# Optimization experiments

Hardware: AMD Instinct MI355X
Metric: run time of the kernel (lower is better)

Reference implementation:

```python
import jax, jax.numpy as jnp
import numpy as np


def setup_inputs() -> dict:
    key = jax.random.key(0)
    ks = jax.random.split(key, 6)
    B, S, D_IN, D_OUT, E, R = 4, 2048, 4096, 4096, 8, 16
    x = jax.random.normal(ks[0], (B, S, D_IN), dtype=jnp.float32)
    probs = jax.random.uniform(ks[1], (B, E), dtype=jnp.float32)
    router_probs = probs / jnp.sum(probs, axis=-1, keepdims=True)
    weight = jax.random.normal(ks[2], (D_OUT, D_IN), dtype=jnp.float32) * 0.02
    bias = jax.random.normal(ks[3], (D_OUT,), dtype=jnp.float32) * 0.02
    lora_A = jax.random.normal(ks[4], (E, R, D_IN), dtype=jnp.float32) * 0.02
    lora_B = jax.random.normal(ks[5], (E, D_OUT, R), dtype=jnp.float32) * 0.02
    return {"x": x, "router_probs": router_probs, "weight": weight,
            "bias": bias, "lora_A": lora_A, "lora_B": lora_B}


def reference(x, router_probs, weight, bias, lora_A, lora_B):
    scaling = 2.0
    # base linear: [b,s,i] @ [o,i]^T + bias
    base_out = jnp.einsum('bsi,oi->bso', x, weight) + bias
    # low-rank per-expert projection: [b,s,e,r] (small: r=16)
    mid = jnp.einsum('bsi,eri->bser', x, lora_A)
    # weight by router probs (per batch, per expert) before up-projection
    mid_w = mid * router_probs[:, None, :, None]
    # sum over experts fused into the up-projection contraction
    delta = jnp.einsum('bser,eor->bso', mid_w, lora_B) * scaling
    return base_out + delta
```

## Files before the change

kernel.cpp:

```cpp
#include <hip/hip_runtime.h>


typedef _Float16 half8 __attribute__((ext_vector_type(8)));
typedef _Float16 half4 __attribute__((ext_vector_type(4)));
typedef float    f32x4 __attribute__((ext_vector_type(4)));

#define M_TOT 8192
#define N_TOT 4096
#define K_IN  4096
#define KA    4224
#define NT    66

__device__ __forceinline__ void cvt_store4(_Float16* p, float4 f) {
  half4 h;
  h[0] = (_Float16)f.x; h[1] = (_Float16)f.y;
  h[2] = (_Float16)f.z; h[3] = (_Float16)f.w;
  *(half4*)p = h;
}

template <int LOG2C, int DCOLS>
__global__ __launch_bounds__(256) void convert_f32_f16_t(
    const float* __restrict__ src, _Float16* __restrict__ dst, int total8) {
  for (int i = blockIdx.x * 256 + threadIdx.x; i < total8;
       i += gridDim.x * 256) {
    int base = i << 3;
    int r = base >> LOG2C;
    int c = base & ((1 << LOG2C) - 1);
    const float4* s = (const float4*)(src + (size_t)base);
    float4 f0 = s[0], f1 = s[1];
    half8 h;
    h[0]=(_Float16)f0.x; h[1]=(_Float16)f0.y; h[2]=(_Float16)f0.z; h[3]=(_Float16)f0.w;
    h[4]=(_Float16)f1.x; h[5]=(_Float16)f1.y; h[6]=(_Float16)f1.z; h[7]=(_Float16)f1.w;
    *(half8*)(dst + (size_t)r * DCOLS + c) = h;
  }
}

__global__ __launch_bounds__(256) void wtail_gather_f16(
    const float* __restrict__ loraB, _Float16* __restrict__ Wa) {
  int idx = blockIdx.x * 256 + threadIdx.x;
  int n = idx >> 7, j = idx & 127;
  int e = j >> 4, r = j & 15;
  Wa[(size_t)n * KA + K_IN + j] =
      (_Float16)loraB[((size_t)e * N_TOT + n) * 16 + r];
}

__global__ __launch_bounds__(256) void lorabf_gather_f32(
    const float* __restrict__ loraB, float* __restrict__ lorabf) {
  int idx = blockIdx.x * 256 + threadIdx.x;
  int n = idx >> 7, j = idx & 127;
  int e = j >> 4, r = j & 15;
  lorabf[(size_t)n * 128 + j] = loraB[((size_t)e * N_TOT + n) * 16 + r];
}

__global__ __launch_bounds__(256) void mid2_kernel(
    _Float16* __restrict__ Xa, const _Float16* __restrict__ lAh,
    const float* __restrict__ router) {
  __shared__ _Float16 As[32 * 64];
  __shared__ _Float16 Bs[128 * 64];
  int tid = threadIdx.x, lane = tid & 63, w = tid >> 6;
  int m0 = blockIdx.x * 32;
  int b = m0 >> 11;
  f32x4 acc[2][2] = {};

  for (int ks = 0; ks < 64; ++ks) {
    int kb = ks * 128;
    {
      const char* s = (const char*)Xa +
          (size_t)(m0 + w * 8 + (lane >> 3)) * (KA * 2) + kb + (lane & 7) * 16;
      __builtin_amdgcn_global_load_lds(
          (const __attribute__((address_space(1))) void*)s,
          (__attribute__((address_space(3))) void*)((char*)As + w * 1024), 16, 0, 0);
    }
#pragma unroll
    for (int i = 0; i < 4; ++i) {
      const char* s = (const char*)lAh +
          (size_t)((w * 4 + i) * 8 + (lane >> 3)) * (4096 * 2) + kb + (lane & 7) * 16;
      __builtin_amdgcn_global_load_lds(
          (const __attribute__((address_space(1))) void*)s,
          (__attribute__((address_space(3))) void*)((char*)Bs + (w * 4 + i) * 1024), 16, 0, 0);
    }
    __syncthreads();
#pragma unroll
    for (int kk = 0; kk < 2; ++kk) {
      half8 a[2], bf[2];
#pragma unroll
      for (int mi = 0; mi < 2; ++mi)
        a[mi] = *(const half8*)(As + (mi * 16 + (lane & 15)) * 64 + kk * 32 + (lane >> 4) * 8);
#pragma unroll
      for (int ni = 0; ni < 2; ++ni)
        bf[ni] = *(const half8*)(Bs + (w * 32 + ni * 16 + (lane & 15)) * 64 + kk * 32 + (lane >> 4) * 8);
#pragma unroll
      for (int mi = 0; mi < 2; ++mi)
#pragma unroll
        for (int ni = 0; ni < 2; ++ni)
          acc[mi][ni] = __builtin_amdgcn_mfma_f32_16x16x32_f16(a[mi], bf[ni], acc[mi][ni], 0, 0, 0);
    }
    __syncthreads();
  }

#pragma unroll
  for (int ni = 0; ni < 2; ++ni) {
    int j = w * 32 + ni * 16 + (lane & 15);
    int e = j >> 4;
    float sc = 2.0f * router[b * 8 + e];
#pragma unroll
    for (int mi = 0; mi < 2; ++mi) {
      f32x4 v = acc[mi][ni];
#pragma unroll
      for (int jj = 0; jj < 4; ++jj) {
        int m = m0 + mi * 16 + (lane >> 4) * 4 + jj;
        Xa[(size_t)m * KA + K_IN + j] = (_Float16)(v[jj] * sc);
      }
    }
  }
}

__global__ __launch_bounds__(256) void mid_kernel(
    const float* __restrict__ x, const float* __restrict__ loraA,
    const float* __restrict__ router, float* __restrict__ midw) {
  __shared__ _Float16 As[32 * 64];
  __shared__ _Float16 Bs[128 * 64];
  int tid = threadIdx.x, lane = tid & 63, w = tid >> 6;
  int m0 = blockIdx.x * 32;
  int b = m0 >> 11;
  f32x4 acc[2][2] = {};
  for (int ks = 0; ks < 64; ++ks) {
    int k0 = ks * 64;
#pragma unroll
    for (int it = 0; it < 2; ++it) {
      int idx = tid + it * 256;
      int r = idx >> 4, c4 = idx & 15;
      float4 f = *(const float4*)(x + (size_t)(m0 + r) * K_IN + k0 + c4 * 4);
      cvt_store4(As + r * 64 + c4 * 4, f);
    }
#pragma unroll
    for (int it = 0; it < 8; ++it) {
      int idx = tid + it * 256;
      int r = idx >> 4, c4 = idx & 15;
      float4 f = *(const float4*)(loraA + (size_t)r * K_IN + k0 + c4 * 4);
      cvt_store4(Bs + r * 64 + c4 * 4, f);
    }
    __syncthreads();
#pragma unroll
    for (int kk = 0; kk < 2; ++kk) {
      half8 a[2], bf[2];
#pragma unroll
      for (int mi = 0; mi < 2; ++mi)
        a[mi] = *(const half8*)(As + (mi * 16 + (lane & 15)) * 64 + kk * 32 + (lane >> 4) * 8);
#pragma unroll
      for (int ni = 0; ni < 2; ++ni)
        bf[ni] = *(const half8*)(Bs + (w * 32 + ni * 16 + (lane & 15)) * 64 + kk * 32 + (lane >> 4) * 8);
#pragma unroll
      for (int mi = 0; mi < 2; ++mi)
#pragma unroll
        for (int ni = 0; ni < 2; ++ni)
          acc[mi][ni] = __builtin_amdgcn_mfma_f32_16x16x32_f16(a[mi], bf[ni], acc[mi][ni], 0, 0, 0);
    }
    __syncthreads();
  }
#pragma unroll
  for (int ni = 0; ni < 2; ++ni) {
    int j = w * 32 + ni * 16 + (lane & 15);
    int e = j >> 4;
    float sc = 2.0f * router[b * 8 + e];
#pragma unroll
    for (int mi = 0; mi < 2; ++mi) {
      f32x4 v = acc[mi][ni];
#pragma unroll
      for (int jj = 0; jj < 4; ++jj) {
        int m = m0 + mi * 16 + (lane >> 4) * 4 + jj;
        midw[(size_t)m * 128 + j] = v[jj] * sc;
      }
    }
  }
}

#define BAR   __builtin_amdgcn_s_barrier()
#define PRIO1 __builtin_amdgcn_s_setprio(1)
#define PRIO0 __builtin_amdgcn_s_setprio(0)
#define LGKM0 do { asm volatile("s_waitcnt lgkmcnt(0)" ::: "memory"); \
                   __builtin_amdgcn_sched_barrier(0); } while (0)
#define LGKM8 asm volatile("s_waitcnt lgkmcnt(8)" ::: "memory")
#define VMW4  asm volatile("s_waitcnt vmcnt(4)" ::: "memory")
#define VMW0  asm volatile("s_waitcnt vmcnt(0)" ::: "memory")
#define GLOAD(src, dst) __builtin_amdgcn_global_load_lds( \
    (const __attribute__((address_space(1))) void*)(src), \
    (__attribute__((address_space(3))) void*)(dst), 16, 0, 0)

#define LOAD_A(mb, buf) do { \
  _Pragma("unroll") for (int mi = 0; mi < 4; ++mi) { \
    int row = wm + ((mb) + mi) * 16 + ln15; \
    _Pragma("unroll") for (int kk = 0; kk < 2; ++kk) \
      areg[mi][kk] = *(const half8*)((const char*)(buf) + row * 128 + \
                                     (((kk * 4 + ln4) ^ ln7) * 16)); \
  } } while (0)

#define LOAD_B2(nb, buf) do { \
  _Pragma("unroll") for (int ni = 0; ni < 2; ++ni) { \
    int row = wn + ((nb) + ni) * 16 + ln15; \
    _Pragma("unroll") for (int kk = 0; kk < 2; ++kk) \
      breg[(nb) + ni][kk] = *(const half8*)((const char*)(buf) + row * 128 + \
                                     (((kk * 4 + ln4) ^ ln7) * 16)); \
  } } while (0)

#define MFMA_Q(mb, nb) do { \
  _Pragma("unroll") for (int kk = 0; kk < 2; ++kk) \
    _Pragma("unroll") for (int mi = 0; mi < 4; ++mi) \
      _Pragma("unroll") for (int ni = 0; ni < 2; ++ni) \
        acc[(mb) + mi][(nb) + ni] = __builtin_amdgcn_mfma_f32_16x16x32_f16( \
            areg[mi][kk], breg[(nb) + ni][kk], acc[(mb) + mi][(nb) + ni], 0, 0, 0); \
  } while (0)

__global__ __launch_bounds__(512, 2) void gemm256(
    const _Float16* __restrict__ Xa, const _Float16* __restrict__ Wa,
    const float* __restrict__ bias, float* __restrict__ out) {
  __shared__ _Float16 As[2][256 * 64];
  __shared__ _Float16 Bs[2][256 * 64];

  int tid = threadIdx.x, lane = tid & 63, w = tid >> 6;
  int ln15 = lane & 15, ln4 = lane >> 4, ln7 = lane & 7;
  int wm = (w >> 2) * 128, wn = (w & 3) * 64;

  int bid = blockIdx.x;
  int xcd = bid & 7, idx = bid >> 3;
  int mt = (xcd & 3) * 8 + (idx & 7);
  int nt = (xcd >> 2) * 8 + (idx >> 3);
  int m0 = mt << 8, n0 = nt << 8;

  const char* XpC = (const char*)Xa + (size_t)m0 * (KA * 2);
  const char* WpC = (const char*)Wa + (size_t)n0 * (KA * 2);

  int lrow = lane >> 3;
  int scol = ((lane & 7) ^ lrow) * 16;
  int off[2][2], lds_off[2][2];
#pragma unroll
  for (int h = 0; h < 2; ++h)
#pragma unroll
    for (int j = 0; j < 2; ++j) {
      int rbase = h * 128 + w * 16 + j * 8;
      off[h][j] = (rbase + lrow) * (KA * 2) + scol;
      lds_off[h][j] = rbase * 128;
    }

  f32x4 acc[8][4] = {};
  half8 areg[4][2], breg[4][2];

  {
    char* a0 = (char*)&As[0][0]; char* b0 = (char*)&Bs[0][0];
    char* a1 = (char*)&As[1][0];
    const char* sA1 = XpC + 128;
    GLOAD(XpC + off[0][0], a0 + lds_off[0][0]); GLOAD(XpC + off[0][1], a0 + lds_off[0][1]);
    GLOAD(XpC + off[1][0], a0 + lds_off[1][0]); GLOAD(XpC + off[1][1], a0 + lds_off[1][1]);
    GLOAD(WpC + off[0][0], b0 + lds_off[0][0]); GLOAD(WpC + off[0][1], b0 + lds_off[0][1]);
    GLOAD(WpC + off[1][0], b0 + lds_off[1][0]); GLOAD(WpC + off[1][1], b0 + lds_off[1][1]);
    GLOAD(sA1 + off[0][0], a1 + lds_off[0][0]); GLOAD(sA1 + off[0][1], a1 + lds_off[0][1]);
    GLOAD(sA1 + off[1][0], a1 + lds_off[1][0]); GLOAD(sA1 + off[1][1], a1 + lds_off[1][1]);
    VMW4; BAR;
  }

#pragma unroll 1
  for (int t = 0; t < NT - 2; ++t) {
    const _Float16* cA = As[t & 1];
    const _Float16* cB = Bs[t & 1];
    char* nB = (char*)&Bs[(t + 1) & 1][0];
    char* nA = (char*)&As[t & 1][0];
    const char* sB = WpC + (size_t)(t + 1) * 128;
    const char* sA = XpC + (size_t)(t + 2) * 128;

    LOAD_A(0, cA); LOAD_B2(0, cB);
    GLOAD(sB + off[0][0], nB + lds_off[0][0]); GLOAD(sB + off[0][1], nB + lds_off[0][1]);
    LGKM8; BAR; LGKM0; PRIO1; MFMA_Q(0, 0); PRIO0; BAR;
    LOAD_B2(2, cB);
    GLOAD(sB + off[1][0], nB + lds_off[1][0]); GLOAD(sB + off[1][1], nB + lds_off[1][1]);
    BAR; LGKM0; PRIO1; MFMA_Q(0, 2); PRIO0; BAR;
    LOAD_A(4, cA);
    BAR; LGKM0; PRIO1; MFMA_Q(4, 2); PRIO0; BAR;
    GLOAD(sA + off[0][0], nA + lds_off[0][0]); GLOAD(sA + off[0][1], nA + lds_off[0][1]);
    GLOAD(sA + off[1][0], nA + lds_off[1][0]); GLOAD(sA + off[1][1], nA + lds_off[1][1]);
    BAR; PRIO1; MFMA_Q(4, 0); PRIO0; VMW4; BAR;
  }

  {
    const _Float16* cA = As[0];
    const _Float16* cB = Bs[0];
    char* nB = (char*)&Bs[1][0];
    const char* sB = WpC + (size_t)65 * 128;
    LOAD_A(0, cA); LOAD_B2(0, cB);
    GLOAD(sB + off[0][0], nB + lds_off[0][0]); GLOAD(sB + off[0][1], nB + lds_off[0][1]);
    LGKM8; BAR; LGKM0; PRIO1; MFMA_Q(0, 0); PRIO0; BAR;
    LOAD_B2(2, cB);
    GLOAD(sB + off[1][0], nB + lds_off[1][0]); GLOAD(sB + off[1][1], nB + lds_off[1][1]);
    BAR; LGKM0; PRIO1; MFMA_Q(0, 2); PRIO0; BAR;
    LOAD_A(4, cA);
    BAR; LGKM0; PRIO1; MFMA_Q(4, 2); PRIO0; BAR;
    BAR; PRIO1; MFMA_Q(4, 0); PRIO0; VMW0; BAR;
  }
  {
    const _Float16* cA = As[1];
    const _Float16* cB = Bs[1];
    LOAD_A(0, cA); LOAD_B2(0, cB);
    BAR; LGKM0; PRIO1; MFMA_Q(0, 0); PRIO0; BAR;
    LOAD_B2(2, cB);
    BAR; LGKM0; PRIO1; MFMA_Q(0, 2); PRIO0; BAR;
    LOAD_A(4, cA);
    BAR; LGKM0; PRIO1; MFMA_Q(4, 2); PRIO0; BAR;
    PRIO1; MFMA_Q(4, 0); PRIO0;
  }

#pragma unroll
  for (int ni = 0; ni < 4; ++ni) {
    int n = n0 + wn + ni * 16 + ln15;
    float bz = bias[n];
#pragma unroll
    for (int mi = 0; mi < 8; ++mi) {
      f32x4 v = acc[mi][ni];
      int mb = m0 + wm + mi * 16 + ln4 * 4;
#pragma unroll
      for (int jj = 0; jj < 4; ++jj)
        out[(size_t)(mb + jj) * N_TOT + n] = v[jj] + bz;
    }
  }
}

__global__ __launch_bounds__(256) void gemm_fallback(
    const float* __restrict__ x, const float* __restrict__ wgt,
    const float* __restrict__ midw, const float* __restrict__ lorabf,
    const float* __restrict__ bias, float* __restrict__ out) {
  __shared__ _Float16 As[128 * 64];
  __shared__ _Float16 Bs[128 * 64];
  int tid = threadIdx.x, lane = tid & 63, w = tid >> 6;
  int mt = blockIdx.x & 63, nt = blockIdx.x >> 6;
  int m0 = mt << 7, n0 = nt << 7;
  int wm = (w >> 1) * 64, wn = (w & 1) * 64;
  f32x4 acc[4][4] = {};
  for (int ks = 0; ks < NT; ++ks) {
    int k0 = ks * 64;
    const float *asrc, *bsrc; size_t astr, bstr; int ac, bc;
    if (ks < 64) { asrc = x;    astr = K_IN; ac = k0;        bsrc = wgt;    bstr = K_IN; bc = k0; }
    else         { asrc = midw; astr = 128;  ac = k0 - K_IN; bsrc = lorabf; bstr = 128;  bc = k0 - K_IN; }
#pragma unroll
    for (int it = 0; it < 8; ++it) {
      int idx = tid + it * 256;
      int r = idx >> 4, c4 = idx & 15;
      float4 fa = *(const float4*)(asrc + (size_t)(m0 + r) * astr + ac + c4 * 4);
      cvt_store4(As + r * 64 + c4 * 4, fa);
      float4 fb = *(const float4*)(bsrc + (size_t)(n0 + r) * bstr + bc + c4 * 4);
      cvt_store4(Bs + r * 64 + c4 * 4, fb);
    }
    __syncthreads();
#pragma unroll
    for (int kk = 0; kk < 2; ++kk) {
      half8 a[4], bf[4];
#pragma unroll
      for (int mi = 0; mi < 4; ++mi)
        a[mi] = *(const half8*)(As + (wm + mi * 16 + (lane & 15)) * 64 + kk * 32 + (lane >> 4) * 8);
#pragma unroll
      for (int ni = 0; ni < 4; ++ni)
        bf[ni] = *(const half8*)(Bs + (wn + ni * 16 + (lane & 15)) * 64 + kk * 32 + (lane >> 4) * 8);
#pragma unroll
      for (int mi = 0; mi < 4; ++mi)
#pragma unroll
        for (int ni = 0; ni < 4; ++ni)
          acc[mi][ni] = __builtin_amdgcn_mfma_f32_16x16x32_f16(a[mi], bf[ni], acc[mi][ni], 0, 0, 0);
    }
    __syncthreads();
  }
#pragma unroll
  for (int ni = 0; ni < 4; ++ni) {
    int n = n0 + wn + ni * 16 + (lane & 15);
    float bz = bias[n];
#pragma unroll
    for (int mi = 0; mi < 4; ++mi) {
      f32x4 v = acc[mi][ni];
      int mbase = m0 + wm + mi * 16 + (lane >> 4) * 4;
#pragma unroll
      for (int jj = 0; jj < 4; ++jj)
        out[(size_t)(mbase + jj) * N_TOT + n] = v[jj] + bz;
    }
  }
}

extern "C" void kernel_launch(void* const* d_in, const int* in_sizes, int n_in,
                              void* d_out, int out_size, void* d_ws, size_t ws_size,
                              hipStream_t stream) {
  const float* x      = (const float*)d_in[0];
  const float* router = (const float*)d_in[1];
  const float* wgt    = (const float*)d_in[2];
  const float* bias   = (const float*)d_in[3];
  const float* loraA  = (const float*)d_in[4];
  const float* loraB  = (const float*)d_in[5];
  float* out = (float*)d_out;
  char* ws = (char*)d_ws;

  const size_t XAUG_B = (size_t)M_TOT * KA * 2;
  const size_t WAUG_B = (size_t)N_TOT * KA * 2;
  const size_t LAH_B  = (size_t)128 * K_IN * 2;
  const size_t MIDW_B = (size_t)M_TOT * 128 * 4;
  bool fast = ws_size >= XAUG_B + WAUG_B + LAH_B;

  if (fast) {
    _Float16* Xa  = (_Float16*)ws;
    _Float16* Wa  = (_Float16*)(ws + XAUG_B);
    _Float16* lAh = (_Float16*)(ws + XAUG_B + WAUG_B);
    convert_f32_f16_t<12, KA><<<2048, 256, 0, stream>>>(x,   Xa, M_TOT * K_IN / 8);
    convert_f32_f16_t<12, KA><<<2048, 256, 0, stream>>>(wgt, Wa, N_TOT * K_IN / 8);
    convert_f32_f16_t<12, 4096><<<256, 256, 0, stream>>>(loraA, lAh, 128 * K_IN / 8);
    wtail_gather_f16<<<2048, 256, 0, stream>>>(loraB, Wa);
    mid2_kernel<<<256, 256, 0, stream>>>(Xa, lAh, router);
    gemm256<<<512, 512, 0, stream>>>(Xa, Wa, bias, out);
  } else {
    float* midw   = (float*)ws;
    float* lorabf = (float*)(ws + MIDW_B);
    lorabf_gather_f32<<<2048, 256, 0, stream>>>(loraB, lorabf);
    mid_kernel<<<256, 256, 0, stream>>>(x, loraA, router, midw);
    gemm_fallback<<<2048, 256, 0, stream>>>(x, wgt, midw, lorabf, bias, out);
  }
}
```

Baseline: 384.4 us.

## Replace barrier-interleaved ping-pong schedule with simple double-buffered loop

```diff
diff --git a/kernel.cpp b/kernel.cpp
--- a/kernel.cpp
+++ b/kernel.cpp
@@ -175,40 +175,52 @@
   }
 }
 
-#define BAR   __builtin_amdgcn_s_barrier()
-#define PRIO1 __builtin_amdgcn_s_setprio(1)
-#define PRIO0 __builtin_amdgcn_s_setprio(0)
-#define LGKM0 do { asm volatile("s_waitcnt lgkmcnt(0)" ::: "memory"); \
-                   __builtin_amdgcn_sched_barrier(0); } while (0)
-#define LGKM8 asm volatile("s_waitcnt lgkmcnt(8)" ::: "memory")
-#define VMW4  asm volatile("s_waitcnt vmcnt(4)" ::: "memory")
-#define VMW0  asm volatile("s_waitcnt vmcnt(0)" ::: "memory")
+#define BAR    __builtin_amdgcn_s_barrier()
+#define SCHED0 __builtin_amdgcn_sched_barrier(0)
+#define PRIO1  __builtin_amdgcn_s_setprio(1)
+#define PRIO0  __builtin_amdgcn_s_setprio(0)
+#define VMW0   asm volatile("s_waitcnt vmcnt(0)" ::: "memory")
 #define GLOAD(src, dst) __builtin_amdgcn_global_load_lds( \
     (const __attribute__((address_space(1))) void*)(src), \
     (__attribute__((address_space(3))) void*)(dst), 16, 0, 0)
 
-#define LOAD_A(mb, buf) do { \
+#define READ_A(aF, mb, buf) do { \
   _Pragma("unroll") for (int mi = 0; mi < 4; ++mi) { \
     int row = wm + ((mb) + mi) * 16 + ln15; \
     _Pragma("unroll") for (int kk = 0; kk < 2; ++kk) \
-      areg[mi][kk] = *(const half8*)((const char*)(buf) + row * 128 + \
-                                     (((kk * 4 + ln4) ^ ln7) * 16)); \
+      aF[mi][kk] = *(const half8*)((const char*)(buf) + row * 128 + \
+                                   (((kk * 4 + ln4) ^ ln7) * 16)); \
   } } while (0)
 
-#define LOAD_B2(nb, buf) do { \
+#define READ_B(bF, nb, buf) do { \
   _Pragma("unroll") for (int ni = 0; ni < 2; ++ni) { \
     int row = wn + ((nb) + ni) * 16 + ln15; \
     _Pragma("unroll") for (int kk = 0; kk < 2; ++kk) \
-      breg[(nb) + ni][kk] = *(const half8*)((const char*)(buf) + row * 128 + \
-                                     (((kk * 4 + ln4) ^ ln7) * 16)); \
+      bF[ni][kk] = *(const half8*)((const char*)(buf) + row * 128 + \
+                                   (((kk * 4 + ln4) ^ ln7) * 16)); \
   } } while (0)
 
-#define MFMA_Q(mb, nb) do { \
+#define MFMA_Q(aF, bF, mb, nb) do { \
+  PRIO1; \
   _Pragma("unroll") for (int kk = 0; kk < 2; ++kk) \
     _Pragma("unroll") for (int mi = 0; mi < 4; ++mi) \
       _Pragma("unroll") for (int ni = 0; ni < 2; ++ni) \
         acc[(mb) + mi][(nb) + ni] = __builtin_amdgcn_mfma_f32_16x16x32_f16( \
-            areg[mi][kk], breg[(nb) + ni][kk], acc[(mb) + mi][(nb) + ni], 0, 0, 0); \
+            aF[mi][kk], bF[ni][kk], acc[(mb) + mi][(nb) + ni], 0, 0, 0); \
+  PRIO0; \
+  } while (0)
+
+#define STAGE(tt, bufA, bufB) do { \
+  const char* sA_ = XpC + (size_t)(tt) * 128; \
+  const char* sB_ = WpC + (size_t)(tt) * 128; \
+  GLOAD(sA_ + off[0][0], (char*)(bufA) + lds_off[0][0]); \
+  GLOAD(sA_ + off[0][1], (char*)(bufA) + lds_off[0][1]); \
+  GLOAD(sA_ + off[1][0], (char*)(bufA) + lds_off[1][0]); \
+  GLOAD(sA_ + off[1][1], (char*)(bufA) + lds_off[1][1]); \
+  GLOAD(sB_ + off[0][0], (char*)(bufB) + lds_off[0][0]); \
+  GLOAD(sB_ + off[0][1], (char*)(bufB) + lds_off[0][1]); \
+  GLOAD(sB_ + off[1][0], (char*)(bufB) + lds_off[1][0]); \
+  GLOAD(sB_ + off[1][1], (char*)(bufB) + lds_off[1][1]); \
   } while (0)
 
 __global__ __launch_bounds__(512, 2) void gemm256(
@@ -243,68 +255,27 @@
     }
 
   f32x4 acc[8][4] = {};
-  half8 areg[4][2], breg[4][2];
-
-  {
-    char* a0 = (char*)&As[0][0]; char* b0 = (char*)&Bs[0][0];
-    char* a1 = (char*)&As[1][0];
-    const char* sA1 = XpC + 128;
-    GLOAD(XpC + off[0][0], a0 + lds_off[0][0]); GLOAD(XpC + off[0][1], a0 + lds_off[0][1]);
-    GLOAD(XpC + off[1][0], a0 + lds_off[1][0]); GLOAD(XpC + off[1][1], a0 + lds_off[1][1]);
-    GLOAD(WpC + off[0][0], b0 + lds_off[0][0]); GLOAD(WpC + off[0][1], b0 + lds_off[0][1]);
-    GLOAD(WpC + off[1][0], b0 + lds_off[1][0]); GLOAD(WpC + off[1][1], b0 + lds_off[1][1]);
-    GLOAD(sA1 + off[0][0], a1 + lds_off[0][0]); GLOAD(sA1 + off[0][1], a1 + lds_off[0][1]);
-    GLOAD(sA1 + off[1][0], a1 + lds_off[1][0]); GLOAD(sA1 + off[1][1], a1 + lds_off[1][1]);
-    VMW4; BAR;
-  }
+
+  STAGE(0, &As[0][0], &Bs[0][0]);
+  VMW0; BAR; SCHED0;
 
 #pragma unroll 1
-  for (int t = 0; t < NT - 2; ++t) {
+  for (int t = 0; t < NT; ++t) {
     const _Float16* cA = As[t & 1];
     const _Float16* cB = Bs[t & 1];
-    char* nB = (char*)&Bs[(t + 1) & 1][0];
-    char* nA = (char*)&As[t & 1][0];
-    const char* sB = WpC + (size_t)(t + 1) * 128;
-    const char* sA = XpC + (size_t)(t + 2) * 128;
-
-    LOAD_A(0, cA); LOAD_B2(0, cB);
-    GLOAD(sB + off[0][0], nB + lds_off[0][0]); GLOAD(sB + off[0][1], nB + lds_off[0][1]);
-    LGKM8; BAR; LGKM0; PRIO1; MFMA_Q(0, 0); PRIO0; BAR;
-    LOAD_B2(2, cB);
-    GLOAD(sB + off[1][0], nB + lds_off[1][0]); GLOAD(sB + off[1][1], nB + lds_off[1][1]);
-    BAR; LGKM0; PRIO1; MFMA_Q(0, 2); PRIO0; BAR;
-    LOAD_A(4, cA);
-    BAR; LGKM0; PRIO1; MFMA_Q(4, 2); PRIO0; BAR;
-    GLOAD(sA + off[0][0], nA + lds_off[0][0]); GLOAD(sA + off[0][1], nA + lds_off[0][1]);
-    GLOAD(sA + off[1][0], nA + lds_off[1][0]); GLOAD(sA + off[1][1], nA + lds_off[1][1]);
-    BAR; PRIO1; MFMA_Q(4, 0); PRIO0; VMW4; BAR;
-  }
-
-  {
-    const _Float16* cA = As[0];
-    const _Float16* cB = Bs[0];
-    char* nB = (char*)&Bs[1][0];
-    const char* sB = WpC + (size_t)65 * 128;
-    LOAD_A(0, cA); LOAD_B2(0, cB);
-    GLOAD(sB + off[0][0], nB + lds_off[0][0]); GLOAD(sB + off[0][1], nB + lds_off[0][1]);
-    LGKM8; BAR; LGKM0; PRIO1; MFMA_Q(0, 0); PRIO0; BAR;
-    LOAD_B2(2, cB);
-    GLOAD(sB + off[1][0], nB + lds_off[1][0]); GLOAD(sB + off[1][1], nB + lds_off[1][1]);
-    BAR; LGKM0; PRIO1; MFMA_Q(0, 2); PRIO0; BAR;
-    LOAD_A(4, cA);
-    BAR; LGKM0; PRIO1; MFMA_Q(4, 2); PRIO0; BAR;
-    BAR; PRIO1; MFMA_Q(4, 0); PRIO0; VMW0; BAR;
-  }
-  {
-    const _Float16* cA = As[1];
-    const _Float16* cB = Bs[1];
-    LOAD_A(0, cA); LOAD_B2(0, cB);
-    BAR; LGKM0; PRIO1; MFMA_Q(0, 0); PRIO0; BAR;
-    LOAD_B2(2, cB);
-    BAR; LGKM0; PRIO1; MFMA_Q(0, 2); PRIO0; BAR;
-    LOAD_A(4, cA);
-    BAR; LGKM0; PRIO1; MFMA_Q(4, 2); PRIO0; BAR;
-    PRIO1; MFMA_Q(4, 0); PRIO0;
+    if (t < NT - 1) STAGE(t + 1, &As[(t + 1) & 1][0], &Bs[(t + 1) & 1][0]);
+
+    half8 a0[4][2], a4[4][2], b01[2][2], b23[2][2];
+    READ_A(a0, 0, cA);
+    READ_B(b01, 0, cB);
+    READ_B(b23, 2, cB);
+    MFMA_Q(a0, b01, 0, 0);
+    READ_A(a4, 4, cA);
+    MFMA_Q(a0, b23, 0, 2);
+    MFMA_Q(a4, b23, 4, 2);
+    MFMA_Q(a4, b01, 4, 0);
+
+    if (t < NT - 1) { VMW0; BAR; SCHED0; }
   }
 
 #pragma unroll
```

Measured after the change: 397.8 us. +3.5%, slower.
